# Kernel optimization log

Measured on AMD Instinct MI355X. Metric: run time of the kernel, lower is better.

## Reference

```python
import jax, jax.numpy as jnp
import numpy as np

PC_START = (-51.2, -51.2)
VOXEL = (0.1, 0.1)
OUT_STRIDE = 4
NUM_POINT = 5


def setup_inputs() -> dict:
    key = jax.random.key(0)
    k1, k2, k3, k4, k5 = jax.random.split(key, 5)
    B, N, C, H, W = 4, 512, 256, 256, 256
    feats = jax.random.normal(k1, (B, C, H, W), dtype=jnp.float32)
    xy = jax.random.uniform(k2, (B, N, 2), minval=-45.0, maxval=45.0, dtype=jnp.float32)
    z = jax.random.uniform(k3, (B, N, 1), minval=-2.0, maxval=2.0, dtype=jnp.float32)
    dims = jax.random.uniform(k4, (B, N, 3), minval=1.0, maxval=5.0, dtype=jnp.float32)
    ry = jax.random.uniform(k5, (B, N, 1), minval=-np.pi, maxval=np.pi, dtype=jnp.float32)
    rois = jnp.concatenate([xy, z, dims, ry], axis=-1)  # [B,N,7]
    return {"spatial_features_2d": feats, "rois": rois}


def _corner_box2d(centers, dims, angles):
    # corners_nd order x0y0, x0y1, x1y1, x1y0 (torch [0,1,3,2] reorder), origin 0.5
    corners_norm = jnp.array([[0., 0.], [0., 1.], [1., 1.], [1., 0.]], dtype=centers.dtype) - 0.5
    corners = dims[:, None, :] * corners_norm[None]  # [N,4,2]
    c, s = jnp.cos(angles), jnp.sin(angles)
    # per-box rotation: out[n,i,k] = sum_j corners[n,i,j] * R[n,j,k], R = [[c,-s],[s,c]]
    R = jnp.stack([jnp.stack([c, -s], axis=-1), jnp.stack([s, c], axis=-1)], axis=-2)  # [N,2,2]
    corners = jnp.einsum('nij,njk->nik', corners, R)
    return corners + centers[:, None, :]


def _box_centers(box):
    # box: [N,7] -> points: [5N,3] (center, front, back, left, right midpoints)
    center2d = box[:, :2]
    height = box[:, 2:3]
    dim2d = box[:, 3:5]
    ry = box[:, -1]
    cor = _corner_box2d(center2d, dim2d, ry)  # [N,4,2]
    front = jnp.concatenate([(cor[:, 0] + cor[:, 1]) / 2, height], axis=-1)
    back = jnp.concatenate([(cor[:, 2] + cor[:, 3]) / 2, height], axis=-1)
    left = jnp.concatenate([(cor[:, 0] + cor[:, 3]) / 2, height], axis=-1)
    right = jnp.concatenate([(cor[:, 1] + cor[:, 2]) / 2, height], axis=-1)
    return jnp.concatenate([box[:, :3], front, back, left, right], axis=0)


def _bilinear(im, x, y):
    # im: [H,W,C]; x,y: [P]
    H, W, _ = im.shape
    xf = jnp.floor(x).astype(jnp.int32)
    yf = jnp.floor(y).astype(jnp.int32)
    x0 = jnp.clip(xf, 0, W - 1)
    x1 = jnp.clip(xf + 1, 0, W - 1)
    y0 = jnp.clip(yf, 0, H - 1)
    y1 = jnp.clip(yf + 1, 0, H - 1)
    Ia, Ib, Ic, Id = im[y0, x0], im[y1, x0], im[y0, x1], im[y1, x1]  # [P,C]
    x0f, x1f = x0.astype(x.dtype), x1.astype(x.dtype)
    y0f, y1f = y0.astype(y.dtype), y1.astype(y.dtype)
    wa = (x1f - x) * (y1f - y)
    wb = (x1f - x) * (y - y0f)
    wc = (x - x0f) * (y1f - y)
    wd = (x - x0f) * (y - y0f)
    return Ia * wa[:, None] + Ib * wb[:, None] + Ic * wc[:, None] + Id * wd[:, None]


def reference(spatial_features_2d, rois):
    # spatial_features_2d: [B,C,H,W]; rois: [B,N,7] -> roi_features: [B,N,NUM_POINT*C]
    bev = jnp.transpose(spatial_features_2d, (0, 2, 3, 1))  # [B,H,W,C]

    def per_batch(im, box):
        pts = _box_centers(box)  # [5N,3]
        xs = (pts[:, 0] - PC_START[0]) / VOXEL[0] / OUT_STRIDE
        ys = (pts[:, 1] - PC_START[1]) / VOXEL[1] / OUT_STRIDE
        fm = _bilinear(im, xs, ys)  # [5N,C]
        N = box.shape[0]
        # torch cat of NUM_POINT sections along channel dim == reshape/transpose
        return fm.reshape(NUM_POINT, N, -1).transpose(1, 0, 2).reshape(N, -1)

    return jax.vmap(per_batch)(bev, rois)
```

## Files before the change

kernel.cpp:

```cpp
#include <hip/hip_runtime.h>
#include <math.h>

constexpr int B = 4;
constexpr int N = 512;
constexpr int C = 256;
constexpr int H = 256;
constexpr int W = 256;
constexpr int NPT = 5;
constexpr int PTS = N * NPT;
constexpr int CHUNKS = 8;
constexpr int PCHUNK = PTS / CHUNKS;
constexpr int CG = 4;
constexpr int NCG = C / CG;
constexpr int NBLK = B * NCG * CHUNKS;


__global__ __launch_bounds__(256)
void bev_gather_kernel(const float* __restrict__ feats,
                       const float* __restrict__ rois,
                       float* __restrict__ out)
{
    const int i    = blockIdx.x;
    const int xcd  = i & 7;
    const int k    = i >> 3;
    const int grp  = xcd * 32 + (k & 31);
    const int chunk= k >> 5;
    const int b    = grp >> 6;
    const int cg   = grp & 63;

    const int tid  = threadIdx.x;
    const int wave = tid >> 6;
    const int lane = tid & 63;
    const int c    = cg * CG + wave;

    __shared__ float sxs[PCHUNK];
    __shared__ float sys[PCHUNK];
    __shared__ float svals[PCHUNK][CG + 1];

    const int qbase = chunk * PCHUNK;

    for (int q = tid; q < PCHUNK; q += 256) {
        const int qq = qbase + q;
        const int n  = qq / NPT;
        const int p  = qq - n * NPT;
        const float* roi = rois + ((size_t)b * N + n) * 7;
        const float cx = roi[0], cy = roi[1];
        const float hx = 0.5f * roi[3];
        const float hy = 0.5f * roi[4];
        float si, co;
        sincosf(roi[6], &si, &co);
        float px = cx, py = cy;
        if      (p == 1) { px = cx - hx * co; py = cy + hx * si; }
        else if (p == 2) { px = cx + hx * co; py = cy - hx * si; }
        else if (p == 3) { px = cx - hy * si; py = cy - hy * co; }
        else if (p == 4) { px = cx + hy * si; py = cy + hy * co; }
        sxs[q] = (px + 51.2f) * 2.5f;
        sys[q] = (py + 51.2f) * 2.5f;
    }
    __syncthreads();

    const float* __restrict__ fp = feats + ((size_t)b * C + c) * (H * W);

#pragma unroll
    for (int j = 0; j < PCHUNK / 64; ++j) {
        const int q = j * 64 + lane;
        const float xs = sxs[q];
        const float ys = sys[q];
        const float xf = floorf(xs);
        const float yf = floorf(ys);
        const int xi = (int)xf;
        const int yi = (int)yf;
        const int x0 = min(max(xi, 0), W - 1);
        const int x1 = min(max(xi + 1, 0), W - 1);
        const int y0 = min(max(yi, 0), H - 1);
        const int y1 = min(max(yi + 1, 0), H - 1);

        const float x0f = (float)x0, x1f = (float)x1;
        const float y0f = (float)y0, y1f = (float)y1;
        const float wa = (x1f - xs) * (y1f - ys);
        const float wb = (x1f - xs) * (ys - y0f);
        const float wc = (xs - x0f) * (y1f - ys);
        const float wd = (xs - x0f) * (ys - y0f);

        const float Ia = fp[y0 * W + x0];
        const float Ib = fp[y1 * W + x0];
        const float Ic = fp[y0 * W + x1];
        const float Id = fp[y1 * W + x1];

        svals[q][wave] = Ia * wa + Ib * wb + Ic * wc + Id * wd;
    }
    __syncthreads();

    for (int q = tid; q < PCHUNK; q += 256) {
        const int qq = qbase + q;
        const int n  = qq / NPT;
        const int p  = qq - n * NPT;
        float4 v = make_float4(svals[q][0], svals[q][1], svals[q][2], svals[q][3]);
        float* op = out + (((size_t)(b * N + n) * NPT + p) * C + cg * CG);
        *reinterpret_cast<float4*>(op) = v;
    }
}

extern "C" void kernel_launch(void* const* d_in, const int* in_sizes, int n_in,
                              void* d_out, int out_size, void* d_ws, size_t ws_size,
                              hipStream_t stream) {
    const float* feats = (const float*)d_in[0];
    const float* rois  = (const float*)d_in[1];
    float* out = (float*)d_out;

    bev_gather_kernel<<<dim3(NBLK), dim3(256), 0, stream>>>(feats, rois, out);
}
```

Measured before the change: 367.8 us.

## Bucket sample points by row tile and gather bilinear taps from LDS slabs

Bilinear sampling becomes three kernels: zero the counters, bucket every sample point into an 8-row tile with atomics, then gather. In the gather kernel each block streams a 9-row slab of 4 channels into LDS with coalesced float4 loads and serves that tile's points from shared memory. This replaces scattered 4-byte global gathers, which waste cache-line bandwidth, with a dense sequential read of the feature map. In exchange the whole map is read even for tiles with no points, there are two extra launches and a workspace round trip, and output writes become per-channel scalar stores.

```diff
diff --git a/kernel.cpp b/kernel.cpp
--- a/kernel.cpp
+++ b/kernel.cpp
@@ -8,68 +8,107 @@
 constexpr int W = 256;
 constexpr int NPT = 5;
 constexpr int PTS = N * NPT;
-constexpr int CHUNKS = 8;
-constexpr int PCHUNK = PTS / CHUNKS;
-constexpr int CG = 4;
+
+constexpr int RT  = 8;
+constexpr int NT  = H / RT;
+constexpr int CG  = 4;
 constexpr int NCG = C / CG;
-constexpr int NBLK = B * NCG * CHUNKS;
+constexpr int CAP = PTS;
 
+constexpr size_t REC_OFF = 512;
+
+__device__ __forceinline__ void point_xy(const float* __restrict__ rois,
+                                         int b, int n, int p,
+                                         float& xs, float& ys) {
+    const float* roi = rois + ((size_t)b * N + n) * 7;
+    const float cx = roi[0], cy = roi[1];
+    const float hx = 0.5f * roi[3];
+    const float hy = 0.5f * roi[4];
+    float si, co;
+    sincosf(roi[6], &si, &co);
+    float px = cx, py = cy;
+    if      (p == 1) { px = cx - hx * co; py = cy + hx * si; }
+    else if (p == 2) { px = cx + hx * co; py = cy - hx * si; }
+    else if (p == 3) { px = cx - hy * si; py = cy - hy * co; }
+    else if (p == 4) { px = cx + hy * si; py = cy + hy * co; }
+    xs = (px + 51.2f) * 2.5f;
+    ys = (py + 51.2f) * 2.5f;
+}
+
+__global__ __launch_bounds__(128)
+void k0_zero(unsigned* __restrict__ cnt) {
+    cnt[threadIdx.x] = 0u;
+}
 
 __global__ __launch_bounds__(256)
-void bev_gather_kernel(const float* __restrict__ feats,
-                       const float* __restrict__ rois,
-                       float* __restrict__ out)
-{
-    const int i    = blockIdx.x;
-    const int xcd  = i & 7;
-    const int k    = i >> 3;
-    const int grp  = xcd * 32 + (k & 31);
-    const int chunk= k >> 5;
-    const int b    = grp >> 6;
-    const int cg   = grp & 63;
+void k1_bucket(const float* __restrict__ rois, unsigned char* __restrict__ ws) {
+    const int gid = blockIdx.x * 256 + threadIdx.x;
+    if (gid >= B * PTS) return;
+    const int b  = gid / PTS;
+    const int qq = gid - b * PTS;
+    const int n  = qq / NPT;
+    const int p  = qq - n * NPT;
 
-    const int tid  = threadIdx.x;
-    const int wave = tid >> 6;
-    const int lane = tid & 63;
-    const int c    = cg * CG + wave;
+    float xs, ys;
+    point_xy(rois, b, n, p, xs, ys);
 
-    __shared__ float sxs[PCHUNK];
-    __shared__ float sys[PCHUNK];
-    __shared__ float svals[PCHUNK][CG + 1];
+    const int yi = (int)floorf(ys);
+    const int y0 = min(max(yi, 0), H - 1);
+    const int tile = y0 >> 3;
 
-    const int qbase = chunk * PCHUNK;
+    unsigned* cnt = (unsigned*)ws;
+    const unsigned slot = atomicAdd(&cnt[b * NT + tile], 1u);
+    float4* rec = (float4*)(ws + REC_OFF);
+    float4 r;
+    r.x = __uint_as_float((unsigned)((n << 3) | p));
+    r.y = xs;
+    r.z = ys;
+    r.w = 0.0f;
+    rec[((size_t)(b * NT + tile)) * CAP + slot] = r;
+}
 
-    for (int q = tid; q < PCHUNK; q += 256) {
-        const int qq = qbase + q;
-        const int n  = qq / NPT;
-        const int p  = qq - n * NPT;
-        const float* roi = rois + ((size_t)b * N + n) * 7;
-        const float cx = roi[0], cy = roi[1];
-        const float hx = 0.5f * roi[3];
-        const float hy = 0.5f * roi[4];
-        float si, co;
-        sincosf(roi[6], &si, &co);
-        float px = cx, py = cy;
-        if      (p == 1) { px = cx - hx * co; py = cy + hx * si; }
-        else if (p == 2) { px = cx + hx * co; py = cy - hx * si; }
-        else if (p == 3) { px = cx - hy * si; py = cy - hy * co; }
-        else if (p == 4) { px = cx + hy * si; py = cy + hy * co; }
-        sxs[q] = (px + 51.2f) * 2.5f;
-        sys[q] = (py + 51.2f) * 2.5f;
+constexpr int SLAB = (RT + 1) * W + 8;
+
+__global__ __launch_bounds__(256)
+void k2_gather(const float* __restrict__ feats,
+               const unsigned char* __restrict__ ws,
+               float* __restrict__ out) {
+    const int t  = blockIdx.x;
+    const int cg = blockIdx.y;
+    const int b  = blockIdx.z;
+    const int tid = threadIdx.x;
+
+    __shared__ float lds[CG * SLAB];
+
+    for (int i = tid; i < CG * (RT + 1) * (W / 4); i += 256) {
+        const int ch  = i / ((RT + 1) * (W / 4));
+        const int rem = i - ch * ((RT + 1) * (W / 4));
+        const int r   = rem / (W / 4);
+        const int c4  = rem - r * (W / 4);
+        const int grow = min(t * RT + r, H - 1);
+        const float4 v = *(const float4*)&feats[(((size_t)b * C + cg * CG + ch) * H + grow) * W + c4 * 4];
+        *(float4*)&lds[ch * SLAB + r * W + c4 * 4] = v;
     }
+
+    const unsigned m = ((const unsigned*)ws)[b * NT + t];
+    const float4* rec = (const float4*)(ws + REC_OFF) + (size_t)(b * NT + t) * CAP;
+
     __syncthreads();
 
-    const float* __restrict__ fp = feats + ((size_t)b * C + c) * (H * W);
+    const int ch = tid & 3;
+    const int pi = tid >> 2;
+    const float* slab = lds + ch * SLAB;
 
-#pragma unroll
-    for (int j = 0; j < PCHUNK / 64; ++j) {
-        const int q = j * 64 + lane;
-        const float xs = sxs[q];
-        const float ys = sys[q];
-        const float xf = floorf(xs);
-        const float yf = floorf(ys);
-        const int xi = (int)xf;
-        const int yi = (int)yf;
+    for (unsigned i = pi; i < m; i += 64) {
+        const float4 r4 = rec[i];
+        const unsigned np = __float_as_uint(r4.x);
+        const int n = np >> 3;
+        const int p = np & 7;
+        const float xs = r4.y;
+        const float ys = r4.z;
+
+        const int xi = (int)floorf(xs);
+        const int yi = (int)floorf(ys);
         const int x0 = min(max(xi, 0), W - 1);
         const int x1 = min(max(xi + 1, 0), W - 1);
         const int y0 = min(max(yi, 0), H - 1);
@@ -82,22 +121,16 @@
         const float wc = (xs - x0f) * (y1f - ys);
         const float wd = (xs - x0f) * (ys - y0f);
 
-        const float Ia = fp[y0 * W + x0];
-        const float Ib = fp[y1 * W + x0];
-        const float Ic = fp[y0 * W + x1];
-        const float Id = fp[y1 * W + x1];
+        const int ly0 = y0 - t * RT;
+        const int ly1 = y1 - t * RT;
 
-        svals[q][wave] = Ia * wa + Ib * wb + Ic * wc + Id * wd;
-    }
-    __syncthreads();
+        const float Ia = slab[ly0 * W + x0];
+        const float Ib = slab[ly1 * W + x0];
+        const float Ic = slab[ly0 * W + x1];
+        const float Id = slab[ly1 * W + x1];
 
-    for (int q = tid; q < PCHUNK; q += 256) {
-        const int qq = qbase + q;
-        const int n  = qq / NPT;
-        const int p  = qq - n * NPT;
-        float4 v = make_float4(svals[q][0], svals[q][1], svals[q][2], svals[q][3]);
-        float* op = out + (((size_t)(b * N + n) * NPT + p) * C + cg * CG);
-        *reinterpret_cast<float4*>(op) = v;
+        out[(((size_t)b * N + n) * NPT + p) * C + cg * CG + ch] =
+            Ia * wa + Ib * wb + Ic * wc + Id * wd;
     }
 }
 
@@ -107,6 +140,9 @@
     const float* feats = (const float*)d_in[0];
     const float* rois  = (const float*)d_in[1];
     float* out = (float*)d_out;
+    unsigned char* ws = (unsigned char*)d_ws;
 
-    bev_gather_kernel<<<dim3(NBLK), dim3(256), 0, stream>>>(feats, rois, out);
+    k0_zero<<<1, 128, 0, stream>>>((unsigned*)ws);
+    k1_bucket<<<(B * PTS + 255) / 256, 256, 0, stream>>>(rois, ws);
+    k2_gather<<<dim3(NT, NCG, B), 256, 0, stream>>>(feats, ws, out);
 }
```

After: 375.2 us. 2.0% more time.

## Bin sample points by row tile and bilinear-sample from LDS-staged feature slabs

Applied to the files above, without the earlier changes.

Replaces the per-point random global gathers with a tiled scheme. Each block owns an 8-row tile of four channels. It recomputes all sample positions, keeps in an LDS list only the points whose base row falls in its tile, and stages that tile of rows into LDS with async global-to-LDS loads. Bilinear interpolation then reads from LDS, and points that overflow the list fall back to direct global gathers. This trades scattered, latency-bound global reads for streaming contiguous reads of the whole feature map, at the cost of redundant per-block trig and binning work and higher LDS use per block.

```diff
diff --git a/kernel.cpp b/kernel.cpp
--- a/kernel.cpp
+++ b/kernel.cpp
@@ -8,41 +8,49 @@
 constexpr int W = 256;
 constexpr int NPT = 5;
 constexpr int PTS = N * NPT;
-constexpr int CHUNKS = 8;
-constexpr int PCHUNK = PTS / CHUNKS;
-constexpr int CG = 4;
+
+constexpr int RT  = 8;
+constexpr int NT  = H / RT;
+constexpr int CG  = 4;
 constexpr int NCG = C / CG;
-constexpr int NBLK = B * NCG * CHUNKS;
+constexpr int SLAB = (RT + 1) * W + 8;
+constexpr int CAPL = 768;
 
 
+__device__ __forceinline__ void async16(const float* g, float* l) {
+#if defined(__has_builtin) && __has_builtin(__builtin_amdgcn_global_load_lds)
+    __builtin_amdgcn_global_load_lds(
+        (const __attribute__((address_space(1))) unsigned int*)g,
+        (__attribute__((address_space(3))) unsigned int*)l, 16, 0, 0);
+#else
+    *(float4*)l = *(const float4*)g;
+#endif
+}
+
 __global__ __launch_bounds__(256)
-void bev_gather_kernel(const float* __restrict__ feats,
-                       const float* __restrict__ rois,
-                       float* __restrict__ out)
+void bev_fused(const float* __restrict__ feats,
+               const float* __restrict__ rois,
+               float* __restrict__ out)
 {
-    const int i    = blockIdx.x;
-    const int xcd  = i & 7;
-    const int k    = i >> 3;
-    const int grp  = xcd * 32 + (k & 31);
-    const int chunk= k >> 5;
-    const int b    = grp >> 6;
-    const int cg   = grp & 63;
-
-    const int tid  = threadIdx.x;
+    const int t   = blockIdx.x;
+    const int cg  = blockIdx.y;
+    const int b   = blockIdx.z;
+    const int tid = threadIdx.x;
     const int wave = tid >> 6;
     const int lane = tid & 63;
-    const int c    = cg * CG + wave;
 
-    __shared__ float sxs[PCHUNK];
-    __shared__ float sys[PCHUNK];
-    __shared__ float svals[PCHUNK][CG + 1];
+    __shared__ __align__(16) float slab[CG * SLAB];
+    __shared__ float    lxs[CAPL];
+    __shared__ float    lys[CAPL];
+    __shared__ unsigned lnp[CAPL];
+    __shared__ unsigned lcnt;
 
-    const int qbase = chunk * PCHUNK;
+    if (tid == 0) lcnt = 0u;
+    __syncthreads();
 
-    for (int q = tid; q < PCHUNK; q += 256) {
-        const int qq = qbase + q;
-        const int n  = qq / NPT;
-        const int p  = qq - n * NPT;
+    for (int q = tid; q < PTS; q += 256) {
+        const int n = q / NPT;
+        const int p = q - n * NPT;
         const float* roi = rois + ((size_t)b * N + n) * 7;
         const float cx = roi[0], cy = roi[1];
         const float hx = 0.5f * roi[3];
@@ -50,26 +58,65 @@
         float si, co;
         sincosf(roi[6], &si, &co);
         float px = cx, py = cy;
-        if      (p == 1) { px = cx - hx * co; py = cy + hx * si; }
-        else if (p == 2) { px = cx + hx * co; py = cy - hx * si; }
-        else if (p == 3) { px = cx - hy * si; py = cy - hy * co; }
-        else if (p == 4) { px = cx + hy * si; py = cy + hy * co; }
-        sxs[q] = (px + 51.2f) * 2.5f;
-        sys[q] = (py + 51.2f) * 2.5f;
+        if      (p == 1) { px -= hx * co; py += hx * si; }
+        else if (p == 2) { px += hx * co; py -= hx * si; }
+        else if (p == 3) { px -= hy * si; py -= hy * co; }
+        else if (p == 4) { px += hy * si; py += hy * co; }
+        const float xs = (px + 51.2f) * 2.5f;
+        const float ys = (py + 51.2f) * 2.5f;
+
+        const int yi = (int)floorf(ys);
+        const int y0 = min(max(yi, 0), H - 1);
+        if ((y0 >> 3) != t) continue;
+
+        const unsigned slot = atomicAdd(&lcnt, 1u);
+        if (slot < CAPL) {
+            lxs[slot] = xs; lys[slot] = ys;
+            lnp[slot] = (unsigned)((n << 3) | p);
+        } else {
+            const int xi = (int)floorf(xs);
+            const int x0 = min(max(xi, 0), W - 1);
+            const int x1 = min(max(xi + 1, 0), W - 1);
+            const int y1 = min(max(yi + 1, 0), H - 1);
+            const float x0f = (float)x0, x1f = (float)x1;
+            const float y0f = (float)y0, y1f = (float)y1;
+            const float wa = (x1f - xs) * (y1f - ys);
+            const float wb = (x1f - xs) * (ys - y0f);
+            const float wc = (xs - x0f) * (y1f - ys);
+            const float wd = (xs - x0f) * (ys - y0f);
+            for (int ch = 0; ch < CG; ++ch) {
+                const float* fp = feats + ((size_t)b * C + cg * CG + ch) * (H * W);
+                const float v = fp[y0 * W + x0] * wa + fp[y1 * W + x0] * wb +
+                                fp[y0 * W + x1] * wc + fp[y1 * W + x1] * wd;
+                out[(((size_t)b * N + n) * NPT + p) * C + cg * CG + ch] = v;
+            }
+        }
+    }
+    __syncthreads();
+    const unsigned m = min(lcnt, (unsigned)CAPL);
+    if (m == 0) return;
+
+    const int nrows = (t == NT - 1) ? RT : (RT + 1);
+    {
+        const float* g = feats + (((size_t)b * C + cg * CG + wave) * H + t * RT) * W
+                         + lane * 4;
+        float* l = slab + wave * SLAB;
+        for (int j = 0; j < nrows; ++j)
+            async16(g + j * W, l + j * W);
     }
     __syncthreads();
 
-    const float* __restrict__ fp = feats + ((size_t)b * C + c) * (H * W);
+    const int ch = tid & 3;
+    const int pi = tid >> 2;
+    const float* sl = slab + ch * SLAB;
 
-#pragma unroll
-    for (int j = 0; j < PCHUNK / 64; ++j) {
-        const int q = j * 64 + lane;
-        const float xs = sxs[q];
-        const float ys = sys[q];
-        const float xf = floorf(xs);
-        const float yf = floorf(ys);
-        const int xi = (int)xf;
-        const int yi = (int)yf;
+    for (unsigned i = pi; i < m; i += 64) {
+        const float xs = lxs[i];
+        const float ys = lys[i];
+        const unsigned np = lnp[i];
+
+        const int xi = (int)floorf(xs);
+        const int yi = (int)floorf(ys);
         const int x0 = min(max(xi, 0), W - 1);
         const int x1 = min(max(xi + 1, 0), W - 1);
         const int y0 = min(max(yi, 0), H - 1);
@@ -82,22 +129,13 @@
         const float wc = (xs - x0f) * (y1f - ys);
         const float wd = (xs - x0f) * (ys - y0f);
 
-        const float Ia = fp[y0 * W + x0];
-        const float Ib = fp[y1 * W + x0];
-        const float Ic = fp[y0 * W + x1];
-        const float Id = fp[y1 * W + x1];
+        const int ly0 = y0 - t * RT;
+        const int ly1 = y1 - t * RT;
 
-        svals[q][wave] = Ia * wa + Ib * wb + Ic * wc + Id * wd;
-    }
-    __syncthreads();
+        const float v = sl[ly0 * W + x0] * wa + sl[ly1 * W + x0] * wb +
+                        sl[ly0 * W + x1] * wc + sl[ly1 * W + x1] * wd;
 
-    for (int q = tid; q < PCHUNK; q += 256) {
-        const int qq = qbase + q;
-        const int n  = qq / NPT;
-        const int p  = qq - n * NPT;
-        float4 v = make_float4(svals[q][0], svals[q][1], svals[q][2], svals[q][3]);
-        float* op = out + (((size_t)(b * N + n) * NPT + p) * C + cg * CG);
-        *reinterpret_cast<float4*>(op) = v;
+        out[(((size_t)b * N + (np >> 3)) * NPT + (np & 7)) * C + cg * CG + ch] = v;
     }
 }
 
@@ -108,5 +146,5 @@
     const float* rois  = (const float*)d_in[1];
     float* out = (float*)d_out;
 
-    bev_gather_kernel<<<dim3(NBLK), dim3(256), 0, stream>>>(feats, rois, out);
+    bev_fused<<<dim3(NT, NCG, B), dim3(256), 0, stream>>>(feats, rois, out);
 }
```

After: 376.7 us. 2.4% more time.
